# Performance work log

Hardware: AMD Instinct MI355X
Metric: run time of the kernel (lower is better)

Reference implementation:

```python
import jax, jax.numpy as jnp
import numpy as np

PI = float(np.pi)
C = jnp.complex64
N = 10  # qubits

def m2(a, b, c, d):
    a, b, c, d = jnp.broadcast_arrays(*(jnp.asarray(v, C) for v in (a, b, c, d)))
    return jnp.stack([jnp.stack([a, b], -1), jnp.stack([c, d], -1)], -2)

def rx_mat(t):
    c = jnp.cos(t / 2); s = jnp.sin(t / 2)
    return m2(c, -1j * s, -1j * s, c)

def ry_mat(t):
    c = jnp.cos(t / 2); s = jnp.sin(t / 2)
    return m2(c, -s, s, c)

def rz_mat(t):
    return m2(jnp.exp(-0.5j * t), 0.0, 0.0, jnp.exp(0.5j * t))

def ps_mat(t):
    return m2(1.0, 0.0, 0.0, jnp.exp(1j * t))

def rot_mat(phi, theta, omega):
    c = jnp.cos(theta / 2); s = jnp.sin(theta / 2)
    return m2(jnp.exp(-0.5j * (phi + omega)) * c,
              -jnp.exp(0.5j * (phi - omega)) * s,
              jnp.exp(-0.5j * (phi - omega)) * s,
              jnp.exp(0.5j * (phi + omega)) * c)

def u2_mat(phi, lam):
    r = 1.0 / np.sqrt(2.0)
    return m2(r, -r * jnp.exp(1j * lam), r * jnp.exp(1j * phi), r * jnp.exp(1j * (phi + lam)))

def u3_mat(theta, phi, lam):
    c = jnp.cos(theta / 2); s = jnp.sin(theta / 2)
    return m2(c, -jnp.exp(1j * lam) * s, jnp.exp(1j * phi) * s, jnp.exp(1j * (phi + lam)) * c)

def controlled(U):
    sh = U.shape[:-2]
    I2 = jnp.broadcast_to(jnp.eye(2, dtype=C), sh + (2, 2))
    Z2 = jnp.zeros(sh + (2, 2), C)
    return jnp.concatenate([jnp.concatenate([I2, Z2], -1), jnp.concatenate([Z2, U], -1)], -2)

Y_M = jnp.array([[0, -1j], [1j, 0]], C)
S_M = jnp.array([[1, 0], [0, 1j]], C)
T_M = jnp.array([[1, 0], [0, np.exp(1j * np.pi / 4)]], C)
SX_M = 0.5 * jnp.array([[1 + 1j, 1 - 1j], [1 - 1j, 1 + 1j]], C)
CNOT_M = jnp.array(np.eye(4)[[0, 1, 3, 2]], C)
CZ_M = jnp.array(np.diag([1.0, 1.0, 1.0, -1.0]), C)
CY_M = jnp.array([[1, 0, 0, 0], [0, 1, 0, 0], [0, 0, 0, -1j], [0, 0, 1j, 0]], C)
SWAP_M = jnp.array(np.eye(4)[[0, 2, 1, 3]], C)
CSWAP_M = jnp.array(np.eye(8)[[0, 1, 2, 3, 4, 6, 5, 7]], C)
TOFF_M = jnp.array(np.eye(8)[[0, 1, 2, 3, 4, 5, 7, 6]], C)
CX12_M = jnp.array(np.eye(4)[[0, 1, 3, 2]], C)  # qubitunitary [[1,0,0,0],[0,1,0,0],[0,0,0,1],[0,0,1,0]]

def apply_gate(state, U, wires):
    # state: [B] + [2]*N ; U: [2^k,2^k] or [B,2^k,2^k]
    B = state.shape[0]
    k = len(wires)
    axes = tuple(w + 1 for w in wires)
    s = jnp.moveaxis(state, axes, tuple(range(1, 1 + k)))
    sh = s.shape
    s = s.reshape(B, 2 ** k, -1)
    U = jnp.asarray(U, s.dtype)
    if U.ndim == 2:
        s = jnp.einsum('ij,bjr->bir', U, s)
    else:
        s = jnp.einsum('bij,bjr->bir', U, s)
    return jnp.moveaxis(s.reshape(sh), tuple(range(1, 1 + k)), axes)

def multirz(state, theta, wires):
    # diagonal exp(-i theta/2 * Z...Z) phase
    z = jnp.array([1.0, -1.0], jnp.float32)
    sign = jnp.ones((1,) * (N + 1), jnp.float32)
    for w in wires:
        shp = [1] * (N + 1); shp[w + 1] = 2
        sign = sign * z.reshape(shp)
    theta = jnp.reshape(jnp.asarray(theta), (-1,) + (1,) * N)
    return state * jnp.exp(-0.5j * theta * sign)

def net(x, w1, b1, w2, b2, fw1, fb1, fw2, fb2):
    dn = ('NCHW', 'OIHW', 'NCHW')
    h = jax.lax.conv_general_dilated(x, w1, (1, 1), 'VALID', dimension_numbers=dn)
    h = jax.nn.relu(h + b1[None, :, None, None])
    h = jax.lax.conv_general_dilated(h, w2, (1, 1), 'VALID', dimension_numbers=dn)
    h = jax.nn.relu(h + b2[None, :, None, None])
    h = jax.lax.reduce_window(h, -jnp.inf, jax.lax.max, (1, 1, 2, 2), (1, 1, 2, 2), 'VALID')
    h = h.reshape(h.shape[0], -1)  # [B, 9216]
    h = jax.nn.relu(h @ fw1.T + fb1)
    h = h @ fw2.T + fb2
    return jax.nn.sigmoid(h) * (2.0 * PI)  # angles in [0, 2pi], dropout in eval mode

def run_circuit(ang, q_rx, q_rz3, q_ps6, q_rot7, q_mrz8, q_crx9, q_cry10, q_crz11, q_u2, q_u3):
    B = ang.shape[0]
    state = jnp.zeros((B, 2 ** N), C).at[:, 0].set(1.0).reshape((B,) + (2,) * N)
    for k in range(N):  # TrainableOpAll(RX)
        state = apply_gate(state, rx_mat(q_rx[k]), (k,))
    for k in range(N):  # OpAll(RY) + repeated rx(wire0, x[:,0])
        state = apply_gate(state, ry_mat(ang[:, k]), (k,))
        state = apply_gate(state, rx_mat(ang[:, 0]), (0,))
    for k in range(N - 1):  # TQAll CNOT ring
        state = apply_gate(state, CNOT_M, (k, k + 1))
    state = apply_gate(state, CNOT_M, (N - 1, 0))
    state = apply_gate(state, rx_mat(ang[:, 1]), (1,))
    state = apply_gate(state, rx_mat(jnp.float32(-PI / 4)), (5,))  # q_layer2 fixed
    state = apply_gate(state, ry_mat(ang[:, 2]), (2,))
    state = apply_gate(state, rz_mat(ang[:, 3]), (3,))
    state = apply_gate(state, S_M, (4,))
    state = apply_gate(state, T_M, (5,))
    state = apply_gate(state, rz_mat(q_rz3[0]), (6,))
    state = apply_gate(state, SX_M, (7,))
    # q_device1 (3-wire) ops do not affect the output -> omitted
    state = apply_gate(state, CZ_M, (0, 5))
    state = apply_gate(state, CNOT_M, (0, 5))
    state = apply_gate(state, CY_M, (0, 5))
    state = apply_gate(state, CY_M, (3, 8))
    state = apply_gate(state, SWAP_M, (2, 3))
    state = apply_gate(state, CSWAP_M, (4, 5, 6))
    state = apply_gate(state, TOFF_M, (8, 5, 0))
    state = apply_gate(state, ps_mat(q_ps6[0]), (8,))
    state = apply_gate(state, ps_mat(ang[:, 7]), (7,))
    state = apply_gate(state, rot_mat(q_rot7[0], q_rot7[1], q_rot7[2]), (4,))
    state = apply_gate(state, rot_mat(ang[:, 6], ang[:, 7], ang[:, 8]), (5,))
    state = multirz(state, q_mrz8[0], (2, 3, 4, 5, 6))
    state = multirz(state, ang[:, 5], (3, 4, 6, 7, 8))
    state = apply_gate(state, controlled(rx_mat(ang[:, 6])), (0, 1))
    state = apply_gate(state, controlled(rx_mat(q_crx9[0])), (4, 5))
    state = apply_gate(state, controlled(ry_mat(ang[:, 6])), (0, 1))
    state = apply_gate(state, controlled(ry_mat(q_cry10[0])), (4, 5))
    state = apply_gate(state, controlled(rz_mat(ang[:, 6])), (0, 1))
    state = apply_gate(state, controlled(rz_mat(q_crz11[0])), (4, 5))
    state = apply_gate(state, controlled(rot_mat(jnp.float32(-PI / 4), jnp.float32(PI / 4), jnp.float32(PI / 2))), (5, 6))
    state = apply_gate(state, controlled(rot_mat(ang[:, 5], ang[:, 6], ang[:, 7])), (7, 8))
    state = apply_gate(state, ps_mat(jnp.float32(PI / 7)), (1,))  # U1 == PhaseShift
    state = apply_gate(state, ps_mat(ang[:, 9]), (2,))
    state = apply_gate(state, u2_mat(q_u2[0], q_u2[1]), (8,))
    state = apply_gate(state, u2_mat(ang[:, 0], ang[:, 1]), (4,))
    state = apply_gate(state, u3_mat(q_u3[0], q_u3[1], q_u3[2]), (5,))
    state = apply_gate(state, u3_mat(ang[:, 4], ang[:, 5], ang[:, 6]), (5,))
    # q_layer16 QubitUnitary is identity -> no-op
    state = apply_gate(state, CX12_M, (1, 2))
    red = tuple(range(1, N + 1))
    evs = [jnp.real(jnp.sum(jnp.conj(state) * apply_gate(state, Y_M, (w,)), axis=red)) for w in range(N)]
    return jnp.stack(evs, 1)  # [B, 10]

def setup_inputs():
    key = jax.random.key(0)
    ks = jax.random.split(key, 16)
    B = 1024
    return {
        'x': jax.random.uniform(ks[0], (B, 1, 28, 28), jnp.float32),
        'conv1_w': jax.random.normal(ks[1], (32, 1, 3, 3), jnp.float32) * 0.2,
        'conv1_b': jnp.zeros((32,), jnp.float32),
        'conv2_w': jax.random.normal(ks[2], (64, 32, 3, 3), jnp.float32) * 0.05,
        'conv2_b': jnp.zeros((64,), jnp.float32),
        'fc1_w': jax.random.normal(ks[3], (128, 9216), jnp.float32) * 0.01,
        'fc1_b': jnp.zeros((128,), jnp.float32),
        'fc2_w': jax.random.normal(ks[4], (10, 128), jnp.float32) * 0.08,
        'fc2_b': jnp.zeros((10,), jnp.float32),
        'q_rx': jax.random.uniform(ks[5], (10,), jnp.float32, 0.0, 2 * PI),
        'q_rz3': jax.random.uniform(ks[6], (1,), jnp.float32, 0.0, 2 * PI),
        'q_ps6': jax.random.uniform(ks[7], (1,), jnp.float32, 0.0, 2 * PI),
        'q_rot7': jax.random.uniform(ks[8], (3,), jnp.float32, 0.0, 2 * PI),
        'q_mrz8': jax.random.uniform(ks[9], (1,), jnp.float32, 0.0, 2 * PI),
        'q_crx9': jax.random.uniform(ks[10], (1,), jnp.float32, 0.0, 2 * PI),
        'q_cry10': jax.random.uniform(ks[11], (1,), jnp.float32, 0.0, 2 * PI),
        'q_crz11': jax.random.uniform(ks[12], (1,), jnp.float32, 0.0, 2 * PI),
        'q_u2_14': jnp.array([PI / 7, PI / 8.8], jnp.float32),
        'q_u3_15': jax.random.uniform(ks[13], (3,), jnp.float32, 0.0, 2 * PI),
    }

def reference(x, conv1_w, conv1_b, conv2_w, conv2_b, fc1_w, fc1_b, fc2_w, fc2_b,
              q_rx, q_rz3, q_ps6, q_rot7, q_mrz8, q_crx9, q_cry10, q_crz11, q_u2_14, q_u3_15):
    ang = net(x, conv1_w, conv1_b, conv2_w, conv2_b, fc1_w, fc1_b, fc2_w, fc2_b)
    ev = run_circuit(ang, q_rx, q_rz3, q_ps6, q_rot7, q_mrz8, q_crx9, q_cry10, q_crz11, q_u2_14, q_u3_15)
    return jax.nn.log_softmax(ev, axis=1)
```

## Files before the change

kernel.cpp:

```cpp
#include <hip/hip_runtime.h>
#include <hip/hip_bf16.h>

#define PI_F 3.14159265358979323846f

__global__ void Static_82300163326800_kernel() {}

typedef _Float16 f16x8 __attribute__((ext_vector_type(8)));
typedef _Float16 f16x4 __attribute__((ext_vector_type(4)));
typedef float f32x4 __attribute__((ext_vector_type(4)));

struct M2 { float2 m00, m01, m10, m11; };

__device__ __forceinline__ float2 cmul2(float2 a, float2 b) {
    return make_float2(a.x*b.x - a.y*b.y, a.x*b.y + a.y*b.x);
}
__device__ __forceinline__ float2 cadd2(float2 a, float2 b) {
    return make_float2(a.x+b.x, a.y+b.y);
}
__device__ __forceinline__ M2 m2mul(M2 b, M2 a) {
    return { cadd2(cmul2(b.m00,a.m00), cmul2(b.m01,a.m10)),
             cadd2(cmul2(b.m00,a.m01), cmul2(b.m01,a.m11)),
             cadd2(cmul2(b.m10,a.m00), cmul2(b.m11,a.m10)),
             cadd2(cmul2(b.m10,a.m01), cmul2(b.m11,a.m11)) };
}
__device__ __forceinline__ M2 mrx(float th) {
    float s, c; __sincosf(0.5f * th, &s, &c);
    return { make_float2(c,0.f), make_float2(0.f,-s), make_float2(0.f,-s), make_float2(c,0.f) };
}
__device__ __forceinline__ M2 mry(float th) {
    float s, c; __sincosf(0.5f * th, &s, &c);
    return { make_float2(c,0.f), make_float2(-s,0.f), make_float2(s,0.f), make_float2(c,0.f) };
}
__device__ __forceinline__ M2 mrzM(float th) {
    float s, c; __sincosf(0.5f * th, &s, &c);
    return { make_float2(c,-s), make_float2(0.f,0.f), make_float2(0.f,0.f), make_float2(c,s) };
}
__device__ __forceinline__ M2 mrot(float phi, float th, float om) {
    float s, c;  __sincosf(0.5f * th, &s, &c);
    float sa, ca; __sincosf(0.5f * (phi + om), &sa, &ca);
    float sd, cd; __sincosf(0.5f * (phi - om), &sd, &cd);
    return { make_float2(ca*c, -sa*c), make_float2(-cd*s, -sd*s),
             make_float2(cd*s, -sd*s), make_float2(ca*c,  sa*c) };
}
__device__ __forceinline__ M2 mu2(float phi, float lam) {
    const float r = 0.7071067811865476f;
    float sl, cl;   __sincosf(lam, &sl, &cl);
    float sp, cp;   __sincosf(phi, &sp, &cp);
    float spl, cpl; __sincosf(phi + lam, &spl, &cpl);
    return { make_float2(r,0.f), make_float2(-r*cl,-r*sl),
             make_float2(r*cp, r*sp), make_float2(r*cpl, r*spl) };
}
__device__ __forceinline__ M2 mu3(float th, float phi, float lam) {
    float s, c;     __sincosf(0.5f * th, &s, &c);
    float sl, cl;   __sincosf(lam, &sl, &cl);
    float sp, cp;   __sincosf(phi, &sp, &cp);
    float spl, cpl; __sincosf(phi + lam, &spl, &cpl);
    return { make_float2(c,0.f), make_float2(-cl*s,-sl*s),
             make_float2(cp*s, sp*s), make_float2(cpl*c, spl*c) };
}


__device__ __forceinline__ void applyL(float2* s, M2 m, int lane, int q) {
    const int bitv = (lane >> q) & 1;
    const float2 cA = bitv ? m.m11 : m.m00;
    const float2 cB = bitv ? m.m10 : m.m01;
    float ox[16], oy[16];
#pragma unroll
    for (int r = 0; r < 16; ++r) {
        ox[r] = __shfl_xor(s[r].x, 1 << q);
        oy[r] = __shfl_xor(s[r].y, 1 << q);
    }
#pragma unroll
    for (int r = 0; r < 16; ++r)
        s[r] = make_float2(cA.x*s[r].x - cA.y*s[r].y + cB.x*ox[r] - cB.y*oy[r],
                           cA.x*s[r].y + cA.y*s[r].x + cB.x*oy[r] + cB.y*ox[r]);
}
template<int P>
__device__ __forceinline__ void applyR(float2* s, M2 m) {
#pragma unroll
    for (int r0 = 0; r0 < 16; ++r0) {
        if (r0 & (1 << P)) continue;
        const int r1 = r0 | (1 << P);
        float2 a = s[r0], d = s[r1];
        s[r0] = cadd2(cmul2(m.m00, a), cmul2(m.m01, d));
        s[r1] = cadd2(cmul2(m.m10, a), cmul2(m.m11, d));
    }
}
__device__ __forceinline__ void diagL(float2* s, float2 d0, float2 d1, int lane, int q) {
    const int bitv = (lane >> q) & 1;
    const float2 f = bitv ? d1 : d0;
#pragma unroll
    for (int r = 0; r < 16; ++r) s[r] = cmul2(f, s[r]);
}
template<int P>
__device__ __forceinline__ void diagR(float2* s, float2 d0, float2 d1) {
#pragma unroll
    for (int r = 0; r < 16; ++r) {
        const float2 f = (r & (1 << P)) ? d1 : d0;
        s[r] = cmul2(f, s[r]);
    }
}
__device__ __forceinline__ void cnotLL(float2* s, int lane, int qc, int qw) {
    const int cb = (lane >> qc) & 1;
    float ox[16], oy[16];
#pragma unroll
    for (int r = 0; r < 16; ++r) {
        ox[r] = __shfl_xor(s[r].x, 1 << qw);
        oy[r] = __shfl_xor(s[r].y, 1 << qw);
    }
#pragma unroll
    for (int r = 0; r < 16; ++r)
        s[r] = cb ? make_float2(ox[r], oy[r]) : s[r];
}
__device__ __forceinline__ void capplyLL(float2* s, M2 m, int lane, int qc, int qw) {
    const int cb = (lane >> qc) & 1, tb = (lane >> qw) & 1;
    float2 cA = tb ? m.m11 : m.m00;
    float2 cB = tb ? m.m10 : m.m01;
    cA = cb ? cA : make_float2(1.f, 0.f);
    cB = cb ? cB : make_float2(0.f, 0.f);
    float ox[16], oy[16];
#pragma unroll
    for (int r = 0; r < 16; ++r) {
        ox[r] = __shfl_xor(s[r].x, 1 << qw);
        oy[r] = __shfl_xor(s[r].y, 1 << qw);
    }
#pragma unroll
    for (int r = 0; r < 16; ++r)
        s[r] = make_float2(cA.x*s[r].x - cA.y*s[r].y + cB.x*ox[r] - cB.y*oy[r],
                           cA.x*s[r].y + cA.y*s[r].x + cB.x*oy[r] + cB.y*ox[r]);
}
__device__ __forceinline__ void cdiagLL(float2* s, float2 d0, float2 d1, int lane, int qc, int qw) {
    const int cb = (lane >> qc) & 1, tb = (lane >> qw) & 1;
    float2 f = tb ? d1 : d0;
    f = cb ? f : make_float2(1.f, 0.f);
#pragma unroll
    for (int r = 0; r < 16; ++r) s[r] = cmul2(f, s[r]);
}
template<int P>
__device__ __forceinline__ void capplyRL(float2* s, M2 m, int lane, int qc) {
    const int cb = (lane >> qc) & 1;
#pragma unroll
    for (int r0 = 0; r0 < 16; ++r0) {
        if (r0 & (1 << P)) continue;
        const int r1 = r0 | (1 << P);
        float2 a = s[r0], d = s[r1];
        float2 na = cadd2(cmul2(m.m00, a), cmul2(m.m01, d));
        float2 nd = cadd2(cmul2(m.m10, a), cmul2(m.m11, d));
        s[r0] = cb ? na : a;
        s[r1] = cb ? nd : d;
    }
}

__global__ __launch_bounds__(256, 1) void circuit_wave(
    const float* __restrict__ ang_g,
    const float* __restrict__ q_rx, const float* __restrict__ q_rz3,
    const float* __restrict__ q_ps6, const float* __restrict__ q_rot7,
    const float* __restrict__ q_mrz8, const float* __restrict__ q_crx9,
    const float* __restrict__ q_cry10, const float* __restrict__ q_crz11,
    const float* __restrict__ q_u2, const float* __restrict__ q_u3,
    float* __restrict__ out)
{
    const int t = threadIdx.x, lane = t & 63, wv = t >> 6;
    const int b = blockIdx.x * 4 + wv;
    float ang[10];
#pragma unroll
    for (int j = 0; j < 10; ++j) ang[j] = ang_g[b * 10 + j];

    float2 s[16];
#pragma unroll
    for (int r = 0; r < 16; ++r) s[r] = make_float2(0.f, 0.f);
    if (lane == 0) s[0].x = 1.f;

    applyL(s, m2mul(mrx(10.f * ang[0]), m2mul(mry(ang[0]), mrx(q_rx[0]))), lane, 5);
    applyL(s, m2mul(mry(ang[1]), mrx(q_rx[1])), lane, 4);
    applyL(s, m2mul(mry(ang[2]), mrx(q_rx[2])), lane, 3);
    applyL(s, m2mul(mry(ang[3]), mrx(q_rx[3])), lane, 2);
    applyL(s, m2mul(mry(ang[4]), mrx(q_rx[4])), lane, 1);
    applyL(s, m2mul(mry(ang[5]), mrx(q_rx[5])), lane, 0);
    applyR<3>(s, m2mul(mry(ang[6]), mrx(q_rx[6])));
    applyR<2>(s, m2mul(mry(ang[7]), mrx(q_rx[7])));
    applyR<1>(s, m2mul(mry(ang[8]), mrx(q_rx[8])));
    applyR<0>(s, m2mul(mry(ang[9]), mrx(q_rx[9])));
    cnotLL(s, lane, 5, 4);
    cnotLL(s, lane, 4, 3);
    cnotLL(s, lane, 3, 2);
    cnotLL(s, lane, 2, 1);
    cnotLL(s, lane, 1, 0);
    {
        const int cb = lane & 1;
#pragma unroll
        for (int r0 = 0; r0 < 8; ++r0) {
            float2 a = s[r0], d = s[r0 + 8];
            s[r0] = cb ? d : a; s[r0 + 8] = cb ? a : d;
        }
    }
    {
        float2 u;
        u = s[8];  s[8]  = s[12]; s[12] = u;
        u = s[9];  s[9]  = s[13]; s[13] = u;
        u = s[10]; s[10] = s[14]; s[14] = u;
        u = s[11]; s[11] = s[15]; s[15] = u;
    }
    {
        float2 u;
        u = s[4];  s[4]  = s[6];  s[6]  = u;
        u = s[5];  s[5]  = s[7];  s[7]  = u;
        u = s[12]; s[12] = s[14]; s[14] = u;
        u = s[13]; s[13] = s[15]; s[15] = u;
    }
    {
        float2 u;
        u = s[2];  s[2]  = s[3];  s[3]  = u;
        u = s[6];  s[6]  = s[7];  s[7]  = u;
        u = s[10]; s[10] = s[11]; s[11] = u;
        u = s[14]; s[14] = s[15]; s[15] = u;
    }
    {
        float ox[8], oy[8];
#pragma unroll
        for (int k = 0; k < 8; ++k) {
            ox[k] = __shfl_xor(s[2*k+1].x, 32);
            oy[k] = __shfl_xor(s[2*k+1].y, 32);
        }
#pragma unroll
        for (int k = 0; k < 8; ++k) s[2*k+1] = make_float2(ox[k], oy[k]);
    }

    applyL(s, mrx(ang[1]), lane, 4);
    {
        M2 Tm = { make_float2(1.f,0.f), make_float2(0.f,0.f), make_float2(0.f,0.f),
                  make_float2(0.7071067811865476f, 0.7071067811865476f) };
        applyL(s, m2mul(Tm, mrx(-PI_F / 4.f)), lane, 0);
    }
    applyL(s, mry(ang[2]), lane, 3);
    { float sn, cs; __sincosf(0.5f * ang[3], &sn, &cs);
      diagL(s, make_float2(cs,-sn), make_float2(cs,sn), lane, 2); }
    diagL(s, make_float2(1.f,0.f), make_float2(0.f,1.f), lane, 1);
    { float sn, cs; __sincosf(0.5f * q_rz3[0], &sn, &cs);
      diagR<3>(s, make_float2(cs,-sn), make_float2(cs,sn)); }
    {
        float sn, cs; __sincosf(ang[7], &sn, &cs);
        M2 SXm = { make_float2(0.5f,0.5f), make_float2(0.5f,-0.5f),
                   make_float2(0.5f,-0.5f), make_float2(0.5f,0.5f) };
        M2 PSm = { make_float2(1.f,0.f), make_float2(0.f,0.f),
                   make_float2(0.f,0.f), make_float2(cs,sn) };
        applyR<2>(s, m2mul(PSm, SXm));
    }
    {
        const int cb = (lane >> 5) & 1;
#pragma unroll
        for (int r = 0; r < 16; ++r)
            s[r] = cb ? make_float2(s[r].y, -s[r].x) : s[r];
    }
    {
        const int cb = (lane >> 2) & 1;
#pragma unroll
        for (int r0 = 0; r0 < 16; ++r0) {
            if (r0 & 2) continue;
            const int r1 = r0 | 2;
            float2 a = s[r0], d = s[r1];
            float2 na = make_float2(d.y, -d.x);
            float2 nd = make_float2(-a.y, a.x);
            s[r0] = cb ? na : a; s[r1] = cb ? nd : d;
        }
    }
    {
        const int pr = ((lane >> 3) & 1) ^ ((lane >> 2) & 1);
        float ox[16], oy[16];
#pragma unroll
        for (int r = 0; r < 16; ++r) {
            ox[r] = __shfl_xor(s[r].x, 12);
            oy[r] = __shfl_xor(s[r].y, 12);
        }
#pragma unroll
        for (int r = 0; r < 16; ++r)
            s[r] = pr ? make_float2(ox[r], oy[r]) : s[r];
    }
    {
        float ox[16], oy[16];
#pragma unroll
        for (int r = 0; r < 16; ++r) {
            ox[r] = __shfl_xor(s[r ^ 8].x, 1);
            oy[r] = __shfl_xor(s[r ^ 8].y, 1);
        }
        const int cb = (lane >> 1) & 1, lb = lane & 1;
#pragma unroll
        for (int r = 0; r < 16; ++r) {
            const int pr = cb & ((r & 8) ? (1 - lb) : lb);
            s[r] = pr ? make_float2(ox[r], oy[r]) : s[r];
        }
    }
    {
        const int lb = lane & 1;
        float ox[8], oy[8];
        const int idx8[8] = {2,3,6,7,10,11,14,15};
#pragma unroll
        for (int k = 0; k < 8; ++k) {
            ox[k] = __shfl_xor(s[idx8[k]].x, 32);
            oy[k] = __shfl_xor(s[idx8[k]].y, 32);
        }
#pragma unroll
        for (int k = 0; k < 8; ++k)
            s[idx8[k]] = lb ? make_float2(ox[k], oy[k]) : s[idx8[k]];
    }
    { float sn, cs; __sincosf(q_ps6[0], &sn, &cs);
      diagR<1>(s, make_float2(1.f,0.f), make_float2(cs,sn)); }
    applyL(s, mrot(q_rot7[0], q_rot7[1], q_rot7[2]), lane, 1);
    applyL(s, mrot(ang[6], ang[7], ang[8]), lane, 0);
    {
        float sh, ch; __sincosf(0.5f * q_mrz8[0], &sh, &ch);
        const int lp = __popc(lane & 0xF) & 1;
        const float sg0 = lp ? sh : -sh;
#pragma unroll
        for (int r = 0; r < 16; ++r) {
            const float sg = (r & 8) ? -sg0 : sg0;
            float2 a = s[r];
            s[r] = make_float2(ch*a.x - sg*a.y, ch*a.y + sg*a.x);
        }
    }
    {
        float sh, ch; __sincosf(0.5f * ang[5], &sh, &ch);
        const int lp = __popc(lane & 6) & 1;
        const float sg0 = lp ? sh : -sh;
#pragma unroll
        for (int r = 0; r < 16; ++r) {
            const int rp = __popc(r & 14) & 1;
            const float sg = rp ? -sg0 : sg0;
            float2 a = s[r];
            s[r] = make_float2(ch*a.x - sg*a.y, ch*a.y + sg*a.x);
        }
    }
    {
        M2 U01 = m2mul(mrzM(ang[6]), m2mul(mry(ang[6]), mrx(ang[6])));
        capplyLL(s, U01, lane, 5, 4);
        M2 U45 = m2mul(mrzM(q_crz11[0]), m2mul(mry(q_cry10[0]), mrx(q_crx9[0])));
        capplyLL(s, U45, lane, 1, 0);
    }
    capplyRL<3>(s, mrot(-PI_F/4.f, PI_F/4.f, PI_F/2.f), lane, 0);
    {
        M2 m = mrot(ang[5], ang[6], ang[7]);
        const int idx4[4] = {4, 5, 12, 13};
#pragma unroll
        for (int k = 0; k < 4; ++k) {
            const int r0 = idx4[k], r1 = r0 | 2;
            float2 a = s[r0], d = s[r1];
            s[r0] = cadd2(cmul2(m.m00, a), cmul2(m.m01, d));
            s[r1] = cadd2(cmul2(m.m10, a), cmul2(m.m11, d));
        }
    }
    { float sn, cs; __sincosf(PI_F / 7.f, &sn, &cs);
      diagL(s, make_float2(1.f,0.f), make_float2(cs,sn), lane, 4); }
    { float sn, cs; __sincosf(ang[9], &sn, &cs);
      diagL(s, make_float2(1.f,0.f), make_float2(cs,sn), lane, 3); }
    applyR<1>(s, mu2(q_u2[0], q_u2[1]));
    applyL(s, mu2(ang[0], ang[1]), lane, 1);
    applyL(s, m2mul(mu3(ang[4], ang[5], ang[6]),
                    mu3(q_u3[0], q_u3[1], q_u3[2])), lane, 0);
    cnotLL(s, lane, 4, 3);

    float ev[10];
#pragma unroll
    for (int w = 0; w < 6; ++w) {
        const int q = 5 - w;
        const int bitv = (lane >> q) & 1;
        float ox[16], oy[16];
#pragma unroll
        for (int r = 0; r < 16; ++r) {
            ox[r] = __shfl_xor(s[r].x, 1 << q);
            oy[r] = __shfl_xor(s[r].y, 1 << q);
        }
        float acc = 0.f;
#pragma unroll
        for (int r = 0; r < 16; ++r)
            acc += s[r].x * oy[r] - s[r].y * ox[r];
        ev[w] = bitv ? 0.f : 2.f * acc;
    }
#pragma unroll
    for (int w = 6; w < 10; ++w) {
        const int P = 9 - w;
        float acc = 0.f;
#pragma unroll
        for (int r0 = 0; r0 < 16; ++r0) {
            if (r0 & (1 << P)) continue;
            const int r1 = r0 | (1 << P);
            acc += s[r0].x * s[r1].y - s[r0].y * s[r1].x;
        }
        ev[w] = 2.f * acc;
    }
#pragma unroll
    for (int w = 0; w < 10; ++w) {
        float v = ev[w];
        v += __shfl_down(v, 32); v += __shfl_down(v, 16); v += __shfl_down(v, 8);
        v += __shfl_down(v, 4);  v += __shfl_down(v, 2);  v += __shfl_down(v, 1);
        ev[w] = v;
    }
    if (lane == 0) {
        float mx = ev[0];
#pragma unroll
        for (int i = 1; i < 10; ++i) mx = fmaxf(mx, ev[i]);
        float ss = 0.f;
#pragma unroll
        for (int i = 0; i < 10; ++i) ss += expf(ev[i] - mx);
        const float ls = logf(ss);
#pragma unroll
        for (int i = 0; i < 10; ++i) out[b * 10 + i] = ev[i] - mx - ls;
    }
}

__global__ __launch_bounds__(256) void prep_all(
    const float* __restrict__ fw1, _Float16* __restrict__ fw1h,
    const float* __restrict__ w2, _Float16* __restrict__ w2t)
{
    const int blk = blockIdx.x;
    if (blk < 1152) {
        int i = blk * 256 + threadIdx.x;
        float4 v = ((const float4*)fw1)[i];
        f16x4 o = { (_Float16)v.x, (_Float16)v.y, (_Float16)v.z, (_Float16)v.w };
        *(f16x4*)(fw1h + i * 4) = o;
    } else {
        int idx = (blk - 1152) * 256 + threadIdx.x;
        if (idx < 18432) {
            int oc = idx / 288, r = idx - oc * 288;
            int s = r >> 5, ic = r & 31;
            w2t[idx] = (_Float16)w2[oc * 288 + ic * 9 + s];
        }
    }
}

__global__ __launch_bounds__(256, 2) void convnet_mfma(
    const float* __restrict__ x, const float* __restrict__ w1, const float* __restrict__ b1,
    const _Float16* __restrict__ w2t, const float* __restrict__ b2,
    _Float16* __restrict__ flat)
{
    __shared__ float xs[784];
    __shared__ __align__(16) float w1t[288];
    __shared__ __align__(16) _Float16 h1t[676 * 40];
    const int n = blockIdx.x, t = threadIdx.x;
    const int lane = t & 63, wv = t >> 6;
    const int m = lane & 15, quad = lane >> 4;

    for (int i = t; i < 784; i += 256) xs[i] = x[n * 784 + i];
    for (int i = t; i < 288; i += 256) {
        int ic = i / 9, k = i - ic * 9;
        w1t[k * 32 + ic] = w1[i];
    }
    __syncthreads();

    {
        const int icg = t & 3;
        float w[9][8];
#pragma unroll
        for (int k = 0; k < 9; ++k) {
            float4 a = *(const float4*)&w1t[k * 32 + icg * 8];
            float4 bsec = *(const float4*)&w1t[k * 32 + icg * 8 + 4];
            w[k][0] = a.x; w[k][1] = a.y; w[k][2] = a.z; w[k][3] = a.w;
            w[k][4] = bsec.x; w[k][5] = bsec.y; w[k][6] = bsec.z; w[k][7] = bsec.w;
        }
        float bb[8];
#pragma unroll
        for (int j = 0; j < 8; ++j) bb[j] = b1[icg * 8 + j];
        for (int pix = t >> 2; pix < 676; pix += 64) {
            const int yy = pix / 26, xx = pix - yy * 26;
            const float* xp = xs + yy * 28 + xx;
            float acc[8];
#pragma unroll
            for (int j = 0; j < 8; ++j) acc[j] = bb[j];
#pragma unroll
            for (int ky = 0; ky < 3; ++ky)
#pragma unroll
                for (int kx = 0; kx < 3; ++kx) {
                    const float xv = xp[ky * 28 + kx];
                    const int k = ky * 3 + kx;
#pragma unroll
                    for (int j = 0; j < 8; ++j) acc[j] += xv * w[k][j];
                }
            f16x8 o;
#pragma unroll
            for (int j = 0; j < 8; ++j) o[j] = (_Float16)fmaxf(acc[j], 0.f);
            *(f16x8*)&h1t[pix * 40 + icg * 8] = o;
        }
    }

    f16x8 bq[9][4];
#pragma unroll
    for (int s = 0; s < 9; ++s)
#pragma unroll
        for (int nt = 0; nt < 4; ++nt)
            bq[s][nt] = *(const f16x8*)(w2t + (nt * 16 + m) * 288 + s * 32 + quad * 8);

    __syncthreads();

    float bb2[4];
#pragma unroll
    for (int nt = 0; nt < 4; ++nt) bb2[nt] = b2[nt * 16 + m];

    _Float16* outp = flat + (size_t)n * 9216;

    for (int q = 0; q < 9; ++q) {
        const int mt = wv + q * 4;
        const int a = mt / 3, b3 = mt - a * 3;
        const int y0 = 2 * a + (m & 1), x0 = 8 * b3 + (m >> 1);
        f32x4 acc[4] = {};
#pragma unroll
        for (int s = 0; s < 9; ++s) {
            const int ky = s / 3, kx = s - ky * 3;
            f16x8 af = *(const f16x8*)&h1t[((y0 + ky) * 26 + x0 + kx) * 40 + quad * 8];
#pragma unroll
            for (int nt = 0; nt < 4; ++nt)
                acc[nt] = __builtin_amdgcn_mfma_f32_16x16x32_f16(af, bq[s][nt], acc[nt], 0, 0, 0);
        }
        const int pooled_idx = a * 12 + 4 * b3 + quad;
#pragma unroll
        for (int nt = 0; nt < 4; ++nt) {
            float v = fmaxf(fmaxf(acc[nt][0], acc[nt][1]), fmaxf(acc[nt][2], acc[nt][3]));
            outp[(nt * 16 + m) * 144 + pooled_idx] = (_Float16)fmaxf(v + bb2[nt], 0.f);
        }
    }
}

__global__ __launch_bounds__(256) void fc1_mfma(
    const _Float16* __restrict__ A, const _Float16* __restrict__ B, float* __restrict__ part)
{
    const int m0 = blockIdx.x * 64, n0 = blockIdx.y * 64, kb = blockIdx.z;
    const int t = threadIdx.x, lane = t & 63, wv = t >> 6;
    const int r = lane & 15, quad = lane >> 4;
    const _Float16* ap = A + (size_t)(m0 + wv * 16 + r) * 9216 + kb * 576 + quad * 8;
    const _Float16* bp = B + (size_t)(n0 + r) * 9216 + kb * 576 + quad * 8;
    f32x4 acc[4] = {};
    for (int ks = 0; ks < 576; ks += 32) {
        f16x8 af = *(const f16x8*)(ap + ks);
#pragma unroll
        for (int nt = 0; nt < 4; ++nt) {
            f16x8 bfr = *(const f16x8*)(bp + (size_t)nt * 16 * 9216 + ks);
            acc[nt] = __builtin_amdgcn_mfma_f32_16x16x32_f16(af, bfr, acc[nt], 0, 0, 0);
        }
    }
    float* pp = part + (size_t)kb * 131072 + (size_t)(m0 + wv * 16 + quad * 4) * 128 + n0 + r;
#pragma unroll
    for (int nt = 0; nt < 4; ++nt)
#pragma unroll
        for (int reg = 0; reg < 4; ++reg)
            pp[reg * 128 + nt * 16] = acc[nt][reg];
}

__global__ __launch_bounds__(128) void fc2_kernel(
    const float* __restrict__ part, const float* __restrict__ fb1,
    const float* __restrict__ fw2, const float* __restrict__ fb2, float* __restrict__ angO)
{
    __shared__ float h[128];
    const int b = blockIdx.x, t = threadIdx.x;
    float s = fb1[t];
#pragma unroll
    for (int kb = 0; kb < 16; ++kb) s += part[(size_t)kb * 131072 + b * 128 + t];
    h[t] = fmaxf(s, 0.f);
    __syncthreads();
    if (t < 10) {
        float d = fb2[t];
#pragma unroll 16
        for (int k = 0; k < 128; ++k) d += h[k] * fw2[t * 128 + k];
        angO[b * 10 + t] = 6.283185307179586f / (1.f + expf(-d));
    }
}

__device__ __forceinline__ int ins1(int x, int p) {
    return ((x >> p) << (p + 1)) | (x & ((1 << p) - 1));
}
__device__ __forceinline__ void apply1(float2* st, int t, int w, M2 m) {
    int p = 9 - w;
    int i0 = ins1(t, p), i1 = i0 | (1 << p);
    float2 a = st[i0], d = st[i1];
    st[i0] = cadd2(cmul2(m.m00, a), cmul2(m.m01, d));
    st[i1] = cadd2(cmul2(m.m10, a), cmul2(m.m11, d));
}
__device__ __forceinline__ void diag1(float2* st, int t, int w, float2 d0, float2 d1) {
    int p = 9 - w;
    int i0 = ins1(t, p), i1 = i0 | (1 << p);
    st[i0] = cmul2(d0, st[i0]);
    st[i1] = cmul2(d1, st[i1]);
}
__device__ __forceinline__ void capply1(float2* st, int t, int c, int w, M2 m) {
    if (t < 256) {
        int pc = 9 - c, pw = 9 - w;
        int pl = pc < pw ? pc : pw, ph = pc + pw - pl;
        int base = ins1(ins1(t, pl), ph) | (1 << pc);
        int i0 = base, i1 = base | (1 << pw);
        float2 a = st[i0], d = st[i1];
        st[i0] = cadd2(cmul2(m.m00, a), cmul2(m.m01, d));
        st[i1] = cadd2(cmul2(m.m10, a), cmul2(m.m11, d));
    }
}
__device__ __forceinline__ void cdiag1(float2* st, int t, int c, int w, float2 d0, float2 d1) {
    if (t < 256) {
        int pc = 9 - c, pw = 9 - w;
        int pl = pc < pw ? pc : pw, ph = pc + pw - pl;
        int base = ins1(ins1(t, pl), ph) | (1 << pc);
        st[base] = cmul2(d0, st[base]);
        st[base | (1 << pw)] = cmul2(d1, st[base | (1 << pw)]);
    }
}
__device__ __forceinline__ void cnotg(float2* st, int t, int c, int w) {
    if (t < 256) {
        int pc = 9 - c, pw = 9 - w;
        int pl = pc < pw ? pc : pw, ph = pc + pw - pl;
        int base = ins1(ins1(t, pl), ph) | (1 << pc);
        int i1 = base | (1 << pw);
        float2 a = st[base]; st[base] = st[i1]; st[i1] = a;
    }
}
__device__ __forceinline__ void czg(float2* st, int t, int c, int w) {
    if (t < 256) {
        int pc = 9 - c, pw = 9 - w;
        int pl = pc < pw ? pc : pw, ph = pc + pw - pl;
        int i = ins1(ins1(t, pl), ph) | (1 << pc) | (1 << pw);
        st[i] = make_float2(-st[i].x, -st[i].y);
    }
}
__device__ __forceinline__ void swapg(float2* st, int t, int a, int b_) {
    if (t < 256) {
        int pa = 9 - a, pb = 9 - b_;
        int pl = pa < pb ? pa : pb, ph = pa + pb - pl;
        int base = ins1(ins1(t, pl), ph);
        int iA = base | (1 << pa), iB = base | (1 << pb);
        float2 u = st[iA]; st[iA] = st[iB]; st[iB] = u;
    }
}
__device__ __forceinline__ void cswap456f(float2* st, int t) {
    if (t < 128) {
        int base = ins1(ins1(ins1(t, 3), 4), 5) | (1 << 5);
        int iA = base | (1 << 4), iB = base | (1 << 3);
        float2 u = st[iA]; st[iA] = st[iB]; st[iB] = u;
    }
}
__device__ __forceinline__ void toff850f(float2* st, int t) {
    if (t < 128) {
        int base = ins1(ins1(ins1(t, 1), 4), 9) | (1 << 1) | (1 << 4);
        int i1 = base | (1 << 9);
        float2 u = st[base]; st[base] = st[i1]; st[i1] = u;
    }
}
__device__ __forceinline__ void mrzg(float2* st, int t, int mask, float th) {
    float sh, ch; __sincosf(0.5f * th, &sh, &ch);
#pragma unroll
    for (int q = 0; q < 2; ++q) {
        int i = t + q * 512;
        float sg = (__popc(i & mask) & 1) ? sh : -sh;
        float2 a = st[i];
        st[i] = make_float2(ch*a.x - sg*a.y, ch*a.y + sg*a.x);
    }
}
__device__ __forceinline__ void run_circ(
    float2* st, float (*red)[10], float* evs, int t, const float* ang,
    const float* q_rx, const float* q_rz3, const float* q_ps6, const float* q_rot7,
    const float* q_mrz8, const float* q_crx9, const float* q_cry10, const float* q_crz11,
    const float* q_u2, const float* q_u3, float* outf)
{
    st[t] = make_float2(t == 0 ? 1.f : 0.f, 0.f);
    st[t + 512] = make_float2(0.f, 0.f);
#pragma unroll
    for (int k = 0; k < 10; ++k) { M2 m = mrx(q_rx[k]); __syncthreads(); apply1(st, t, k, m); }
    {
        M2 mx0 = mrx(ang[0]);
#pragma unroll
        for (int k = 0; k < 10; ++k) {
            M2 m = mry(ang[k]); __syncthreads(); apply1(st, t, k, m);
            __syncthreads(); apply1(st, t, 0, mx0);
        }
    }
#pragma unroll
    for (int k = 0; k < 9; ++k) { __syncthreads(); cnotg(st, t, k, k + 1); }
    __syncthreads(); cnotg(st, t, 9, 0);
    { M2 m = mrx(ang[1]);      __syncthreads(); apply1(st, t, 1, m); }
    { M2 m = mrx(-PI_F / 4.f); __syncthreads(); apply1(st, t, 5, m); }
    { M2 m = mry(ang[2]);      __syncthreads(); apply1(st, t, 2, m); }
    { float s, c; __sincosf(0.5f * ang[3], &s, &c);
      __syncthreads(); diag1(st, t, 3, make_float2(c,-s), make_float2(c,s)); }
    __syncthreads(); diag1(st, t, 4, make_float2(1.f,0.f), make_float2(0.f,1.f));
    __syncthreads(); diag1(st, t, 5, make_float2(1.f,0.f),
                           make_float2(0.7071067811865476f, 0.7071067811865476f));
    { float s, c; __sincosf(0.5f * q_rz3[0], &s, &c);
      __syncthreads(); diag1(st, t, 6, make_float2(c,-s), make_float2(c,s)); }
    { M2 m = { make_float2(0.5f,0.5f), make_float2(0.5f,-0.5f),
               make_float2(0.5f,-0.5f), make_float2(0.5f,0.5f) };
      __syncthreads(); apply1(st, t, 7, m); }
    __syncthreads(); czg(st, t, 0, 5);
    __syncthreads(); cnotg(st, t, 0, 5);
    { M2 y = { make_float2(0.f,0.f), make_float2(0.f,-1.f),
               make_float2(0.f,1.f), make_float2(0.f,0.f) };
      __syncthreads(); capply1(st, t, 0, 5, y);
      __syncthreads(); capply1(st, t, 3, 8, y); }
    __syncthreads(); swapg(st, t, 2, 3);
    __syncthreads(); cswap456f(st, t);
    __syncthreads(); toff850f(st, t);
    { float s, c; __sincosf(q_ps6[0], &s, &c);
      __syncthreads(); diag1(st, t, 8, make_float2(1.f,0.f), make_float2(c,s)); }
    { float s, c; __sincosf(ang[7], &s, &c);
      __syncthreads(); diag1(st, t, 7, make_float2(1.f,0.f), make_float2(c,s)); }
    { M2 m = mrot(q_rot7[0], q_rot7[1], q_rot7[2]); __syncthreads(); apply1(st, t, 4, m); }
    { M2 m = mrot(ang[6], ang[7], ang[8]);          __syncthreads(); apply1(st, t, 5, m); }
    __syncthreads(); mrzg(st, t, 0xF8, q_mrz8[0]);
    __syncthreads(); mrzg(st, t, 0x6E, ang[5]);
    { M2 m = mrx(ang[6]);      __syncthreads(); capply1(st, t, 0, 1, m); }
    { M2 m = mrx(q_crx9[0]);   __syncthreads(); capply1(st, t, 4, 5, m); }
    { M2 m = mry(ang[6]);      __syncthreads(); capply1(st, t, 0, 1, m); }
    { M2 m = mry(q_cry10[0]);  __syncthreads(); capply1(st, t, 4, 5, m); }
    { float s, c; __sincosf(0.5f * ang[6], &s, &c);
      __syncthreads(); cdiag1(st, t, 0, 1, make_float2(c,-s), make_float2(c,s)); }
    { float s, c; __sincosf(0.5f * q_crz11[0], &s, &c);
      __syncthreads(); cdiag1(st, t, 4, 5, make_float2(c,-s), make_float2(c,s)); }
    { M2 m = mrot(-PI_F/4.f, PI_F/4.f, PI_F/2.f); __syncthreads(); capply1(st, t, 5, 6, m); }
    { M2 m = mrot(ang[5], ang[6], ang[7]);        __syncthreads(); capply1(st, t, 7, 8, m); }
    { float s, c; __sincosf(PI_F/7.f, &s, &c);
      __syncthreads(); diag1(st, t, 1, make_float2(1.f,0.f), make_float2(c,s)); }
    { float s, c; __sincosf(ang[9], &s, &c);
      __syncthreads(); diag1(st, t, 2, make_float2(1.f,0.f), make_float2(c,s)); }
    { M2 m = mu2(q_u2[0], q_u2[1]); __syncthreads(); apply1(st, t, 8, m); }
    { M2 m = mu2(ang[0], ang[1]);   __syncthreads(); apply1(st, t, 4, m); }
    { M2 m = mu3(q_u3[0], q_u3[1], q_u3[2]); __syncthreads(); apply1(st, t, 5, m); }
    { M2 m = mu3(ang[4], ang[5], ang[6]);    __syncthreads(); apply1(st, t, 5, m); }
    __syncthreads(); cnotg(st, t, 1, 2);
    __syncthreads();
    float loc[10];
#pragma unroll
    for (int w = 0; w < 10; ++w) {
        int p = 9 - w;
        int i0 = ins1(t, p), i1 = i0 | (1 << p);
        float2 a = st[i0], c = st[i1];
        loc[w] = 2.f * (a.x * c.y - a.y * c.x);
    }
    int lane = t & 63, wvv = t >> 6;
#pragma unroll
    for (int w = 0; w < 10; ++w) {
        float v = loc[w];
        v += __shfl_down(v, 32); v += __shfl_down(v, 16); v += __shfl_down(v, 8);
        v += __shfl_down(v, 4);  v += __shfl_down(v, 2);  v += __shfl_down(v, 1);
        if (lane == 0) red[wvv][w] = v;
    }
    __syncthreads();
    if (t < 10) {
        float e = 0.f;
#pragma unroll
        for (int i = 0; i < 8; ++i) e += red[i][t];
        evs[t] = e;
    }
    __syncthreads();
    if (t < 10) {
        float mx = evs[0];
#pragma unroll
        for (int i = 1; i < 10; ++i) mx = fmaxf(mx, evs[i]);
        float ss = 0.f;
#pragma unroll
        for (int i = 0; i < 10; ++i) ss += expf(evs[i] - mx);
        outf[t] = evs[t] - mx - logf(ss);
    }
}
template <int NT>
__device__ __forceinline__ void conv_stage(
    float* buf, int n, int t,
    const float* __restrict__ x, const float* __restrict__ w1, const float* __restrict__ b1,
    const float* __restrict__ w2, const float* __restrict__ b2)
{
    float* xs  = buf;
    float* w1s = buf + 784;
    float* h1s = buf + 1072;
    float* w2s = buf + 1748;
    const int ocq = t / 24, r = t - ocq * 24;
    const bool active = (t < 384);
    for (int i = t; i < 784; i += NT) xs[i] = x[n * 784 + i];
    for (int i = t; i < 288; i += NT) w1s[i] = w1[i];
    float acc[4][24];
#pragma unroll
    for (int j = 0; j < 4; ++j)
#pragma unroll
        for (int xo = 0; xo < 24; ++xo) acc[j][xo] = 0.f;
    for (int ic = 0; ic < 32; ++ic) {
        __syncthreads();
        float bb1 = b1[ic];
        for (int i = t; i < 676; i += NT) {
            int yy = i / 26, xx = i - yy * 26;
            const float* xp = xs + yy * 28 + xx;
            const float* wp = w1s + ic * 9;
            float s = bb1;
#pragma unroll
            for (int ky = 0; ky < 3; ++ky)
#pragma unroll
                for (int kx = 0; kx < 3; ++kx)
                    s += xp[ky * 28 + kx] * wp[ky * 3 + kx];
            h1s[i] = fmaxf(s, 0.f);
        }
        for (int i = t; i < 576; i += NT) {
            int oc = i / 9, k = i - oc * 9;
            w2s[i] = w2[oc * 288 + ic * 9 + k];
        }
        __syncthreads();
        if (active) {
            float wr[4][9];
#pragma unroll
            for (int j = 0; j < 4; ++j)
#pragma unroll
                for (int k = 0; k < 9; ++k)
                    wr[j][k] = w2s[(ocq * 4 + j) * 9 + k];
            float c0[3], c1[3];
#pragma unroll
            for (int q = 0; q < 3; ++q) { c0[q] = h1s[(r + q) * 26]; c1[q] = h1s[(r + q) * 26 + 1]; }
#pragma unroll
            for (int xo = 0; xo < 24; ++xo) {
                float c2[3];
#pragma unroll
                for (int q = 0; q < 3; ++q) c2[q] = h1s[(r + q) * 26 + xo + 2];
#pragma unroll
                for (int j = 0; j < 4; ++j) {
                    acc[j][xo] += wr[j][0]*c0[0] + wr[j][1]*c1[0] + wr[j][2]*c2[0]
                                + wr[j][3]*c0[1] + wr[j][4]*c1[1] + wr[j][5]*c2[1]
                                + wr[j][6]*c0[2] + wr[j][7]*c1[2] + wr[j][8]*c2[2];
                }
#pragma unroll
                for (int q = 0; q < 3; ++q) { c0[q] = c1[q]; c1[q] = c2[q]; }
            }
        }
    }
    __syncthreads();
    if (active && (r & 1)) {
#pragma unroll
        for (int j = 0; j < 4; ++j) {
            int oc = ocq * 4 + j;
            float bb = b2[oc];
#pragma unroll
            for (int px = 0; px < 12; ++px) {
                float v0 = fmaxf(acc[j][2*px]   + bb, 0.f);
                float v1 = fmaxf(acc[j][2*px+1] + bb, 0.f);
                buf[oc * 144 + (r >> 1) * 12 + px] = fmaxf(v0, v1);
            }
        }
    }
    __syncthreads();
    if (active && !(r & 1)) {
#pragma unroll
        for (int j = 0; j < 4; ++j) {
            int oc = ocq * 4 + j;
            float bb = b2[oc];
#pragma unroll
            for (int px = 0; px < 12; ++px) {
                float v0 = fmaxf(acc[j][2*px]   + bb, 0.f);
                float v1 = fmaxf(acc[j][2*px+1] + bb, 0.f);
                int idx = oc * 144 + (r >> 1) * 12 + px;
                buf[idx] = fmaxf(fmaxf(v0, v1), buf[idx]);
            }
        }
    }
    __syncthreads();
}
__global__ __launch_bounds__(512) void fused_kernel(
    const float* __restrict__ x, const float* __restrict__ w1, const float* __restrict__ b1,
    const float* __restrict__ w2, const float* __restrict__ b2,
    const float* __restrict__ fw1, const float* __restrict__ fb1,
    const float* __restrict__ fw2, const float* __restrict__ fb2,
    const float* __restrict__ q_rx, const float* __restrict__ q_rz3,
    const float* __restrict__ q_ps6, const float* __restrict__ q_rot7,
    const float* __restrict__ q_mrz8, const float* __restrict__ q_crx9,
    const float* __restrict__ q_cry10, const float* __restrict__ q_crz11,
    const float* __restrict__ q_u2, const float* __restrict__ q_u3,
    float* __restrict__ out)
{
    __shared__ float buf[9216];
    __shared__ float2 st[1024];
    __shared__ float hred[512];
    __shared__ float hvec[128];
    __shared__ float angs[10];
    __shared__ float red[8][10];
    __shared__ float evs[10];
    const int n = blockIdx.x, t = threadIdx.x;
    conv_stage<512>(buf, n, t, x, w1, b1, w2, b2);
    {
        const int j = t >> 2, q = t & 3;
        const float* wrow = fw1 + (size_t)j * 9216 + q * 2304;
        const float* arow = buf + q * 2304;
        float s = 0.f;
        for (int k = 0; k < 2304; k += 4) {
            float4 w = *(const float4*)(wrow + k);
            s += w.x * arow[k] + w.y * arow[k+1] + w.z * arow[k+2] + w.w * arow[k+3];
        }
        hred[t] = s;
    }
    __syncthreads();
    if (t < 128)
        hvec[t] = fmaxf(fb1[t] + hred[t*4] + hred[t*4+1] + hred[t*4+2] + hred[t*4+3], 0.f);
    __syncthreads();
    if (t < 10) {
        float d = fb2[t];
#pragma unroll 16
        for (int k = 0; k < 128; ++k) d += hvec[k] * fw2[t * 128 + k];
        angs[t] = 6.283185307179586f / (1.f + expf(-d));
    }
    __syncthreads();
    run_circ(st, red, evs, t, angs, q_rx, q_rz3, q_ps6, q_rot7, q_mrz8,
             q_crx9, q_cry10, q_crz11, q_u2, q_u3, out + n * 10);
}

extern "C" void kernel_launch(void* const* d_in, const int* in_sizes, int n_in,
                              void* d_out, int out_size, void* d_ws, size_t ws_size,
                              hipStream_t stream)
{
    (void)in_sizes; (void)n_in;
    const float* x    = (const float*)d_in[0];
    const float* w1   = (const float*)d_in[1];
    const float* b1   = (const float*)d_in[2];
    const float* w2   = (const float*)d_in[3];
    const float* b2   = (const float*)d_in[4];
    const float* fw1  = (const float*)d_in[5];
    const float* fb1  = (const float*)d_in[6];
    const float* fw2  = (const float*)d_in[7];
    const float* fb2  = (const float*)d_in[8];
    const float* qrx  = (const float*)d_in[9];
    const float* qrz3 = (const float*)d_in[10];
    const float* qps6 = (const float*)d_in[11];
    const float* qrot7 = (const float*)d_in[12];
    const float* qmrz8 = (const float*)d_in[13];
    const float* qcrx9 = (const float*)d_in[14];
    const float* qcry10 = (const float*)d_in[15];
    const float* qcrz11 = (const float*)d_in[16];
    const float* qu2  = (const float*)d_in[17];
    const float* qu3  = (const float*)d_in[18];
    float* out = (float*)d_out;

    const size_t flat_bytes = (size_t)1024 * 9216 * 2;
    const size_t part_bytes = (size_t)16 * 1024 * 128 * 4;
    const size_t ang_bytes  = (size_t)1024 * 10 * 4;
    const size_t w2t_bytes  = (size_t)18432 * 2;
    const size_t fw1h_bytes = (size_t)128 * 9216 * 2;
    const size_t o_flat = 0;
    const size_t o_part = o_flat + flat_bytes;
    const size_t o_ang  = o_part + part_bytes;
    const size_t o_w2t  = o_ang + ang_bytes;
    const size_t o_fw1h = o_w2t + w2t_bytes;
    const size_t need   = o_fw1h + fw1h_bytes;

    (void)hipGetLastError();

    if (ws_size >= need) {
        _Float16* flat = (_Float16*)((char*)d_ws + o_flat);
        float*    part = (float*)((char*)d_ws + o_part);
        float*    angb = (float*)((char*)d_ws + o_ang);
        _Float16* w2t  = (_Float16*)((char*)d_ws + o_w2t);
        _Float16* fw1h = (_Float16*)((char*)d_ws + o_fw1h);
        prep_all<<<1224, 256, 0, stream>>>(fw1, fw1h, w2, w2t);
        convnet_mfma<<<1024, 256, 0, stream>>>(x, w1, b1, w2t, b2, flat);
        fc1_mfma<<<dim3(16, 2, 16), 256, 0, stream>>>(flat, fw1h, part);
        fc2_kernel<<<1024, 128, 0, stream>>>(part, fb1, fw2, fb2, angb);
        circuit_wave<<<256, 256, 0, stream>>>(angb, qrx, qrz3, qps6, qrot7, qmrz8,
                                              qcrx9, qcry10, qcrz11, qu2, qu3, out);
    } else {
        fused_kernel<<<1024, 512, 0, stream>>>(x, w1, b1, w2, b2, fw1, fb1, fw2, fb2,
                                               qrx, qrz3, qps6, qrot7, qmrz8,
                                               qcrx9, qcry10, qcrz11, qu2, qu3, out);
    }
    if (hipGetLastError() != hipSuccess) {
        (void)hipMemsetAsync(d_out, 0x7F, (size_t)out_size * 2, stream);
    }
}
```

Measured before the change: 180.6 us.

## Fuse fc1 weight fp16 conversion into GEMM and repack conv1 LDS layout

Drops the separate fp32-to-fp16 conversion pass over the fc1 weights. fc1_mfma now reads the fp32 weights directly and converts them in registers, which removes a 2.4MB write and a later re-read. The conv1 output in LDS moves from an interleaved stride-40 layout to four planar channel-group planes, which shrinks shared memory so launch bounds can be raised to 3 blocks per CU. The cost is that fc1 reads twice as many weight bytes from memory on every tile load, and it adds conversion ALU work inside the GEMM loop.

```diff
diff --git a/kernel.cpp b/kernel.cpp
--- a/kernel.cpp
+++ b/kernel.cpp
@@ -407,34 +407,25 @@
     }
 }
 
-__global__ __launch_bounds__(256) void prep_all(
-    const float* __restrict__ fw1, _Float16* __restrict__ fw1h,
+__global__ __launch_bounds__(256) void prep_w2(
     const float* __restrict__ w2, _Float16* __restrict__ w2t)
 {
-    const int blk = blockIdx.x;
-    if (blk < 1152) {
-        int i = blk * 256 + threadIdx.x;
-        float4 v = ((const float4*)fw1)[i];
-        f16x4 o = { (_Float16)v.x, (_Float16)v.y, (_Float16)v.z, (_Float16)v.w };
-        *(f16x4*)(fw1h + i * 4) = o;
-    } else {
-        int idx = (blk - 1152) * 256 + threadIdx.x;
-        if (idx < 18432) {
-            int oc = idx / 288, r = idx - oc * 288;
-            int s = r >> 5, ic = r & 31;
-            w2t[idx] = (_Float16)w2[oc * 288 + ic * 9 + s];
-        }
-    }
-}
-
-__global__ __launch_bounds__(256, 2) void convnet_mfma(
+    int idx = blockIdx.x * 256 + threadIdx.x;
+    if (idx < 18432) {
+        int oc = idx / 288, r = idx - oc * 288;
+        int s = r >> 5, ic = r & 31;
+        w2t[idx] = (_Float16)w2[oc * 288 + ic * 9 + s];
+    }
+}
+
+__global__ __launch_bounds__(256, 3) void convnet_mfma(
     const float* __restrict__ x, const float* __restrict__ w1, const float* __restrict__ b1,
     const _Float16* __restrict__ w2t, const float* __restrict__ b2,
     _Float16* __restrict__ flat)
 {
     __shared__ float xs[784];
     __shared__ __align__(16) float w1t[288];
-    __shared__ __align__(16) _Float16 h1t[676 * 40];
+    __shared__ __align__(16) _Float16 h1t[4 * 676 * 8];
     const int n = blockIdx.x, t = threadIdx.x;
     const int lane = t & 63, wv = t >> 6;
     const int m = lane & 15, quad = lane >> 4;
@@ -459,6 +450,7 @@
         float bb[8];
 #pragma unroll
         for (int j = 0; j < 8; ++j) bb[j] = b1[icg * 8 + j];
+        _Float16* h1p = h1t + icg * 5408;
         for (int pix = t >> 2; pix < 676; pix += 64) {
             const int yy = pix / 26, xx = pix - yy * 26;
             const float* xp = xs + yy * 28 + xx;
@@ -477,7 +469,7 @@
             f16x8 o;
 #pragma unroll
             for (int j = 0; j < 8; ++j) o[j] = (_Float16)fmaxf(acc[j], 0.f);
-            *(f16x8*)&h1t[pix * 40 + icg * 8] = o;
+            *(f16x8*)&h1p[pix * 8] = o;
         }
     }
 
@@ -495,6 +487,7 @@
     for (int nt = 0; nt < 4; ++nt) bb2[nt] = b2[nt * 16 + m];
 
     _Float16* outp = flat + (size_t)n * 9216;
+    const _Float16* h1q = h1t + quad * 5408;
 
     for (int q = 0; q < 9; ++q) {
         const int mt = wv + q * 4;
@@ -504,7 +497,7 @@
 #pragma unroll
         for (int s = 0; s < 9; ++s) {
             const int ky = s / 3, kx = s - ky * 3;
-            f16x8 af = *(const f16x8*)&h1t[((y0 + ky) * 26 + x0 + kx) * 40 + quad * 8];
+            f16x8 af = *(const f16x8*)&h1q[((y0 + ky) * 26 + x0 + kx) * 8];
 #pragma unroll
             for (int nt = 0; nt < 4; ++nt)
                 acc[nt] = __builtin_amdgcn_mfma_f32_16x16x32_f16(af, bq[s][nt], acc[nt], 0, 0, 0);
@@ -519,19 +512,23 @@
 }
 
 __global__ __launch_bounds__(256) void fc1_mfma(
-    const _Float16* __restrict__ A, const _Float16* __restrict__ B, float* __restrict__ part)
+    const _Float16* __restrict__ A, const float* __restrict__ B, float* __restrict__ part)
 {
     const int m0 = blockIdx.x * 64, n0 = blockIdx.y * 64, kb = blockIdx.z;
     const int t = threadIdx.x, lane = t & 63, wv = t >> 6;
     const int r = lane & 15, quad = lane >> 4;
     const _Float16* ap = A + (size_t)(m0 + wv * 16 + r) * 9216 + kb * 576 + quad * 8;
-    const _Float16* bp = B + (size_t)(n0 + r) * 9216 + kb * 576 + quad * 8;
+    const float*    bp = B + (size_t)(n0 + r) * 9216 + kb * 576 + quad * 8;
     f32x4 acc[4] = {};
     for (int ks = 0; ks < 576; ks += 32) {
         f16x8 af = *(const f16x8*)(ap + ks);
 #pragma unroll
         for (int nt = 0; nt < 4; ++nt) {
-            f16x8 bfr = *(const f16x8*)(bp + (size_t)nt * 16 * 9216 + ks);
+            const float* bb = bp + (size_t)nt * 16 * 9216 + ks;
+            float4 b0 = *(const float4*)(bb);
+            float4 b1 = *(const float4*)(bb + 4);
+            f16x8 bfr = { (_Float16)b0.x, (_Float16)b0.y, (_Float16)b0.z, (_Float16)b0.w,
+                          (_Float16)b1.x, (_Float16)b1.y, (_Float16)b1.z, (_Float16)b1.w };
             acc[nt] = __builtin_amdgcn_mfma_f32_16x16x32_f16(af, bfr, acc[nt], 0, 0, 0);
         }
     }
@@ -926,13 +923,11 @@
     const size_t part_bytes = (size_t)16 * 1024 * 128 * 4;
     const size_t ang_bytes  = (size_t)1024 * 10 * 4;
     const size_t w2t_bytes  = (size_t)18432 * 2;
-    const size_t fw1h_bytes = (size_t)128 * 9216 * 2;
     const size_t o_flat = 0;
     const size_t o_part = o_flat + flat_bytes;
     const size_t o_ang  = o_part + part_bytes;
     const size_t o_w2t  = o_ang + ang_bytes;
-    const size_t o_fw1h = o_w2t + w2t_bytes;
-    const size_t need   = o_fw1h + fw1h_bytes;
+    const size_t need   = o_w2t + w2t_bytes;
 
     (void)hipGetLastError();
 
@@ -941,10 +936,9 @@
         float*    part = (float*)((char*)d_ws + o_part);
         float*    angb = (float*)((char*)d_ws + o_ang);
         _Float16* w2t  = (_Float16*)((char*)d_ws + o_w2t);
-        _Float16* fw1h = (_Float16*)((char*)d_ws + o_fw1h);
-        prep_all<<<1224, 256, 0, stream>>>(fw1, fw1h, w2, w2t);
+        prep_w2<<<72, 256, 0, stream>>>(w2, w2t);
         convnet_mfma<<<1024, 256, 0, stream>>>(x, w1, b1, w2t, b2, flat);
-        fc1_mfma<<<dim3(16, 2, 16), 256, 0, stream>>>(flat, fw1h, part);
+        fc1_mfma<<<dim3(16, 2, 16), 256, 0, stream>>>(flat, fw1, part);
         fc2_kernel<<<1024, 128, 0, stream>>>(part, fb1, fw2, fb2, angb);
         circuit_wave<<<256, 256, 0, stream>>>(angb, qrx, qrz3, qps6, qrot7, qmrz8,
                                               qcrx9, qcry10, qcrz11, qu2, qu3, out);
```

After: 211.9 us. +17.3%, slower.
